# Kernel optimization log

Measured on AMD Instinct MI355X. Metric: run time of the kernel, lower is better.

The kernel has to match this reference:

```python
import jax, jax.numpy as jnp
import numpy as np

COST_CLASS, COST_BBOX, COST_GIOU = 1.0, 5.0, 2.0


def _lsa(cost):
    """Rectangular linear sum assignment (minimize), Jonker-Volgenant style.
    Returns (row_ind, col_ind) like scipy.optimize.linear_sum_assignment."""
    c = np.asarray(cost, dtype=np.float64)
    transposed = c.shape[0] > c.shape[1]
    if transposed:
        c = c.T
    n, m = c.shape  # n <= m
    INF = 1e18
    u = np.zeros(n + 1)
    v = np.zeros(m + 1)
    p = np.zeros(m + 1, dtype=np.int64)   # p[j]: row (1-based) matched to col j, 0 = free
    way = np.zeros(m + 1, dtype=np.int64)
    for i in range(1, n + 1):
        p[0] = i
        j0 = 0
        minv = np.full(m + 1, INF)
        used = np.zeros(m + 1, dtype=bool)
        while True:
            used[j0] = True
            i0 = p[j0]
            cur = c[i0 - 1, :] - u[i0] - v[1:]
            mv = minv[1:]
            upd = (~used[1:]) & (cur < mv)
            mv[upd] = cur[upd]
            way[1:][upd] = j0
            masked = np.where(used[1:], INF, mv)
            j1 = int(np.argmin(masked)) + 1
            delta = masked[j1 - 1]
            u[p[used]] += delta
            v[used] -= delta
            minv[1:][~used[1:]] -= delta
            j0 = j1
            if p[j0] == 0:
                break
        while j0:
            j1 = way[j0]
            p[j0] = p[j1]
            j0 = j1
    rows = p[1:] - 1
    cols = np.arange(m)
    keep = rows >= 0
    ri, ci = rows[keep], cols[keep]
    if transposed:
        ri, ci = ci, ri
    order = np.argsort(ri)
    return ri[order], ci[order]


def _solve_blocks(cost, n_per):
    """cost: np [Q, B*n_per]; solve LSA per diagonal block, return 0/1 solution."""
    Q, T = cost.shape
    B = T // n_per
    sol = np.zeros((Q, T), dtype=np.float32)
    for b in range(B):
        ri, ci = _lsa(cost[:, b * n_per:(b + 1) * n_per])
        sol[ri, b * n_per + ci] = 1.0
    return sol


def box_cxcywh_to_xyxy(b):
    cx, cy, w, h = jnp.split(b, 4, axis=-1)
    return jnp.concatenate([cx - 0.5 * w, cy - 0.5 * h, cx + 0.5 * w, cy + 0.5 * h], axis=-1)


def generalized_box_iou(b1, b2):
    # b1: [N,4] xyxy, b2: [M,4] xyxy -> [N,M]
    area1 = (b1[:, 2] - b1[:, 0]) * (b1[:, 3] - b1[:, 1])
    area2 = (b2[:, 2] - b2[:, 0]) * (b2[:, 3] - b2[:, 1])
    lt = jnp.maximum(b1[:, None, :2], b2[None, :, :2])
    rb = jnp.minimum(b1[:, None, 2:], b2[None, :, 2:])
    wh = jnp.clip(rb - lt, 0.0)
    inter = wh[..., 0] * wh[..., 1]
    union = area1[:, None] + area2[None, :] - inter
    iou = inter / union
    ltc = jnp.minimum(b1[:, None, :2], b2[None, :, :2])
    rbc = jnp.maximum(b1[:, None, 2:], b2[None, :, 2:])
    whc = jnp.clip(rbc - ltc, 0.0)
    areac = whc[..., 0] * whc[..., 1]
    return iou - (areac - union) / areac


def build_cost(pred_logits, pred_boxes, tgt_labels, tgt_boxes, n_per):
    B, Q, C = pred_logits.shape
    out_prob = jax.nn.softmax(pred_logits.reshape(B * Q, C), axis=-1)
    out_bbox = pred_boxes.reshape(B * Q, 4)
    cost_class = -out_prob[:, tgt_labels]                                  # [N,T]
    cost_bbox = jnp.sum(jnp.abs(out_bbox[:, None, :] - tgt_boxes[None, :, :]), axis=-1)  # L1 cdist
    cost_giou = -generalized_box_iou(box_cxcywh_to_xyxy(out_bbox), box_cxcywh_to_xyxy(tgt_boxes))
    cm = COST_BBOX * cost_bbox + COST_CLASS * cost_class + COST_GIOU * cost_giou
    cm = cm.reshape(B, Q, B, n_per)
    blocks = cm[jnp.arange(B), :, jnp.arange(B), :]        # diagonal blocks [B,Q,n_per]
    return jnp.transpose(blocks, (1, 0, 2)).reshape(Q, B * n_per)  # hstack -> [Q, T]


def setup_inputs() -> dict:
    key = jax.random.key(0)
    k1, k2, k3, k4 = jax.random.split(key, 4)
    B, Q, C, n_per = 16, 900, 92, 32
    T = B * n_per
    return {
        "pred_logits": jax.random.normal(k1, (B, Q, C), dtype=jnp.float32),
        "pred_boxes": jax.random.uniform(k2, (B, Q, 4), dtype=jnp.float32),
        "tgt_labels": jax.random.randint(k3, (T,), 0, C, dtype=jnp.int64),
        "tgt_boxes": jax.random.uniform(k4, (T, 4), dtype=jnp.float32),
        "n_targets": n_per,
    }


def reference(pred_logits, pred_boxes, tgt_labels, tgt_boxes, n_targets):
    n_per = int(n_targets)
    cost = build_cost(pred_logits, pred_boxes, tgt_labels, tgt_boxes, n_per)
    sol = jax.pure_callback(
        lambda c: _solve_blocks(np.asarray(c, dtype=np.float64), n_per),
        jax.ShapeDtypeStruct(cost.shape, jnp.float32),
        cost,
    )
    return sol
```

## Files before the change

### kernel.cpp

```cpp
#include <hip/hip_runtime.h>
#include <math.h>

#define BB 16
#define QQ 900
#define CC 92
#define NP 32
#define TT (BB*NP)
#define RSTRIDE 1024
#define NT 512

#define WSC_COST 0
#define WSC_MAX  (BB*NP*RSTRIDE*4)
#define WSC_SUM  (WSC_MAX + BB*QQ*4)
#define WSC_A    (WSC_SUM + BB*QQ*4)
#define WS_NEED  (WSC_A + TT*4)

__device__ __forceinline__ double mkdbl(int lo, int hi) {
    return __longlong_as_double(((long long)hi << 32) | (unsigned int)lo);
}
__device__ __forceinline__ double readlane_dbl(double x, int s) {
    long long l = __double_as_longlong(x);
    int lo = __builtin_amdgcn_readlane((int)l, s);
    int hi = __builtin_amdgcn_readlane((int)(l >> 32), s);
    return mkdbl(lo, hi);
}
__device__ __forceinline__ double bpermute_dbl(int srclane, double x) {
    long long l = __double_as_longlong(x);
    int lo = __builtin_amdgcn_ds_bpermute(srclane << 2, (int)l);
    int hi = __builtin_amdgcn_ds_bpermute(srclane << 2, (int)(l >> 32));
    return mkdbl(lo, hi);
}

#define DPP_MIN64(CTRL)                                                       \
    {                                                                         \
        long long _l = __double_as_longlong(m);                               \
        int _lo = (int)_l, _hi = (int)(_l >> 32);                             \
        int _olo = __builtin_amdgcn_update_dpp(_lo, _lo, CTRL, 0xf, 0xf, false); \
        int _ohi = __builtin_amdgcn_update_dpp(_hi, _hi, CTRL, 0xf, 0xf, false); \
        m = fmin(m, mkdbl(_olo, _ohi));                                       \
    }

__launch_bounds__(256)
__global__ void denom_kernel(const float* __restrict__ logits,
                             float* __restrict__ wmax,
                             float* __restrict__ wsum)
{
    int idx = blockIdx.x * 256 + threadIdx.x;
    if (idx >= BB * QQ) return;
    const float4* row4 = (const float4*)(logits + (size_t)idx * CC);
    float mx = -INFINITY;
    #pragma unroll
    for (int k = 0; k < 23; ++k) {
        float4 x = row4[k];
        mx = fmaxf(mx, x.x); mx = fmaxf(mx, x.y);
        mx = fmaxf(mx, x.z); mx = fmaxf(mx, x.w);
    }
    float s = 0.f;
    #pragma unroll
    for (int k = 0; k < 23; ++k) {
        float4 x = row4[k];
        s += expf(x.x - mx); s += expf(x.y - mx);
        s += expf(x.z - mx); s += expf(x.w - mx);
    }
    wmax[idx] = mx;
    wsum[idx] = s;
}

__launch_bounds__(256)
__global__ void cost_kernel(const float* __restrict__ logits,
                            const float* __restrict__ pboxes,
                            const int*   __restrict__ labels,
                            const float* __restrict__ tboxes,
                            const float* __restrict__ wmax,
                            const float* __restrict__ wsum,
                            float* __restrict__ wcost)
{
    const int r = blockIdx.x;
    const int b = r >> 5, t = r & 31;
    const float* lg = logits + (size_t)b * QQ * CC;
    const float* pb = pboxes + (size_t)b * QQ * 4;
    const float* tb = tboxes + (size_t)b * NP * 4;
    const float* smax = wmax + b * QQ;
    const float* ssum = wsum + b * QQ;

    const float t0 = tb[t*4+0], t1 = tb[t*4+1], t2 = tb[t*4+2], t3 = tb[t*4+3];
    const int   lt = labels[b * NP + t];
    const float tx1 = t0 - 0.5f*t2, ty1 = t1 - 0.5f*t3;
    const float tx2 = t0 + 0.5f*t2, ty2 = t1 + 0.5f*t3;
    const float area2 = (tx2-tx1)*(ty2-ty1);

    float* crow = wcost + (size_t)r * RSTRIDE;
    for (int q = threadIdx.x; q < RSTRIDE; q += 256) {
        float val = 0.f;
        if (q < QQ) {
            float l    = lg[q * CC + lt];
            float prob = expf(l - smax[q]) / ssum[q];
            float cclass = -prob;
            float p0 = pb[q*4+0], p1 = pb[q*4+1], p2 = pb[q*4+2], p3 = pb[q*4+3];
            float cbbox = fabsf(p0-t0) + fabsf(p1-t1)
                        + fabsf(p2-t2) + fabsf(p3-t3);
            float px1 = p0 - 0.5f*p2, py1 = p1 - 0.5f*p3;
            float px2 = p0 + 0.5f*p2, py2 = p1 + 0.5f*p3;
            float area1 = (px2-px1)*(py2-py1);
            float ltx = fmaxf(px1,tx1), lty = fmaxf(py1,ty1);
            float rbx = fminf(px2,tx2), rby = fminf(py2,ty2);
            float wx = fmaxf(rbx-ltx, 0.f), wy = fmaxf(rby-lty, 0.f);
            float inter = wx*wy;
            float uni = area1 + area2 - inter;
            float iou = inter / uni;
            float cx1 = fminf(px1,tx1), cy1 = fminf(py1,ty1);
            float cx2 = fmaxf(px2,tx2), cy2 = fmaxf(py2,ty2);
            float cwx = fmaxf(cx2-cx1, 0.f), cwy = fmaxf(cy2-cy1, 0.f);
            float areac = cwx*cwy;
            float giou = iou - (areac - uni) / areac;
            val = 5.f*cbbox + 1.f*cclass + 2.f*(-giou);
        }
        crow[q] = val;
    }
}

#define C_OFF_COST 0
#define C_SZ_COST  (NP * RSTRIDE * 4)
#define C_OFF_V    (C_OFF_COST + C_SZ_COST)
#define C_OFF_FLAG (C_OFF_V + 7208)
#define C_OFF_ASN  (C_OFF_FLAG + 128)
#define C_DYN      (C_OFF_ASN + 128)

__launch_bounds__(512)
__global__ void walk_kernel(const float* __restrict__ wcost,
                            float* __restrict__ out)
{
    extern __shared__ char smem[];
    float*  s_cost = (float*)(smem + C_OFF_COST);
    double* s_v    = (double*)(smem + C_OFF_V);
    volatile int* s_flag = (volatile int*)(smem + C_OFF_FLAG);
    int*    s_asn  = (int*)(smem + C_OFF_ASN);

    const int b    = blockIdx.x;
    const int tid  = threadIdx.x;
    const int wv   = tid >> 6;
    const int lane = tid & 63;

    if (tid < 32) s_flag[tid] = 0;
    __syncthreads();

    if (wv != 0) {
        for (int t = wv - 1; t < NP; t += 7) {
            const float4* src =
                (const float4*)(wcost + ((size_t)(b * NP + t) * RSTRIDE));
            float4* dst = (float4*)(s_cost + t * RSTRIDE);
            float4 v0 = src[lane];
            float4 v1 = src[lane + 64];
            float4 v2 = src[lane + 128];
            float4 v3 = src[lane + 192];
            dst[lane]       = v0;
            dst[lane + 64]  = v1;
            dst[lane + 128] = v2;
            dst[lane + 192] = v3;
            asm volatile("s_waitcnt vmcnt(0) lgkmcnt(0)" ::: "memory");
            if (lane == 0) s_flag[t] = 1;
        }
    } else {
        for (int j = lane; j <= QQ; j += 64) s_v[j] = 0.0;
        asm volatile("s_waitcnt lgkmcnt(0)" ::: "memory");

        int acol = 0;
        double ureg = 0.0;
        const float4* cbase4 = (const float4*)s_cost;

        double vreg[16];
        #pragma unroll
        for (int k = 0; k < 16; ++k) {
            int col = 4 * lane + ((k >> 2) << 8) + (k & 3) + 1;
            vreg[k] = (col <= QQ) ? 0.0 : -1.0e300;
        }

        int nv = 0;

        while (nv < 1) {
            if (s_flag[0]) nv = 1;
            else __builtin_amdgcn_s_sleep(2);
        }
        float4 cf[4];
        {
            const float4* crow4 = cbase4;
            #pragma unroll
            for (int k = 0; k < 4; ++k) cf[k] = crow4[lane + (k << 6)];
        }

        for (int i = 1; i <= NP; ++i) {
            int i0 = i, j1prev = 0, T = 0;
            int path_reg = 1, row_reg = 1;

            for (int t = 1;; ++t) {
                if (lane == t) row_reg = i0;
                if (j1prev) {
                    #pragma unroll
                    for (int k = 0; k < 16; ++k) {
                        int col = 4 * lane + ((k >> 2) << 8) + (k & 3) + 1;
                        if (col == j1prev) vreg[k] = -1.0e300;
                    }
                }

                double key[16];
                #pragma unroll
                for (int k = 0; k < 4; ++k) {
                    const float* cp = (const float*)&cf[k];
                    #pragma unroll
                    for (int e2 = 0; e2 < 4; ++e2) {
                        int kk  = 4 * k + e2;
                        int col = 4 * lane + (k << 8) + e2 + 1;
                        double d = (double)cp[e2] - vreg[kk];
                        long long bits =
                            (__double_as_longlong(d) & ~2047LL) | (long long)col;
                        key[kk] = __longlong_as_double(bits);
                    }
                }
                double a0 = fmin(key[0], key[1]),   a1 = fmin(key[2], key[3]);
                double a2 = fmin(key[4], key[5]),   a3 = fmin(key[6], key[7]);
                double a4 = fmin(key[8], key[9]),   a5 = fmin(key[10], key[11]);
                double a6 = fmin(key[12], key[13]), a7 = fmin(key[14], key[15]);
                double b0 = fmin(a0, a1), b1 = fmin(a2, a3);
                double b2 = fmin(a4, a5), b3 = fmin(a6, a7);
                double m  = fmin(fmin(b0, b1), fmin(b2, b3));

                DPP_MIN64(0x111);
                DPP_MIN64(0x112);
                DPP_MIN64(0x114);
                DPP_MIN64(0x118);
                DPP_MIN64(0x142);
                DPP_MIN64(0x143);

                int wlo = __builtin_amdgcn_readlane((int)__double_as_longlong(m), 63);
                int j1  = wlo & 2047;

                if (lane == t) path_reg = j1;

                unsigned long long mask = __ballot(acol == j1);
                if (mask == 0) { T = t; break; }
                int L = (int)__builtin_ctzll(mask);
                i0 = L + 1;
                j1prev = j1;

                const float4* crow4 = cbase4 + (size_t)L * (RSTRIDE / 4);
                #pragma unroll
                for (int k = 0; k < 4; ++k) cf[k] = crow4[lane + (k << 6)];
            }

            bool pre = false;
            if (i < NP) {
                if (nv > i) pre = true;
                else if (s_flag[25] && s_flag[26] && s_flag[27] && s_flag[28]
                      && s_flag[29] && s_flag[30] && s_flag[31]) {
                    nv = NP;
                    pre = true;
                }
                if (pre) {
                    const float4* crow4 = cbase4 + (size_t)i * (RSTRIDE / 4);
                    #pragma unroll
                    for (int k = 0; k < 4; ++k) cf[k] = crow4[lane + (k << 6)];
                }
            }

            const int  rt  = row_reg;
            const int  myj = path_reg;
            const bool act = (lane >= 1 && lane <= T);
            double mydelta = 0.0, vv = 0.0;
            {
                double cD = 0.0, v0j = 0.0;
                if (act) {
                    cD  = (double)s_cost[(rt - 1) * RSTRIDE + (myj - 1)];
                    v0j = s_v[myj];
                }
                double u0rt = bpermute_dbl(rt, ureg);
                if (act) {
                    mydelta = (cD - u0rt) - v0j;
                    vv = v0j;
                }
            }
            bool inpath = false;
            for (int s = 1; s <= T; ++s) {
                double ds = readlane_dbl(mydelta, s);
                int    js = __builtin_amdgcn_readlane(path_reg, s);
                int    rs = __builtin_amdgcn_readlane(row_reg, s);
                if (lane + 1 == rs) inpath = true;
                if (inpath) ureg += ds;
                if (lane >= 1 && lane <  s) vv -= ds;
                if (rs == lane + 1) acol = js;
            }
            if (T > 1) {
                if (act) s_v[myj] = vv;
                for (int s = 1; s <= T; ++s) {
                    int    js  = __builtin_amdgcn_readlane(path_reg, s);
                    double vvs = readlane_dbl(vv, s);
                    #pragma unroll
                    for (int k = 0; k < 16; ++k) {
                        int col = 4 * lane + ((k >> 2) << 8) + (k & 3) + 1;
                        if (col == js) vreg[k] = vvs;
                    }
                }
            }

            if (i < NP && !pre) {
                while (nv <= i) {
                    if (s_flag[nv]) ++nv;
                    else __builtin_amdgcn_s_sleep(2);
                }
                const float4* crow4 = cbase4 + (size_t)i * (RSTRIDE / 4);
                #pragma unroll
                for (int k = 0; k < 4; ++k) cf[k] = crow4[lane + (k << 6)];
            }
        }

        if (lane < NP) s_asn[lane] = acol - 1;
    }
    __syncthreads();

    for (int e = tid; e < QQ * 8; e += 512) {
        int q = e >> 3;
        int f = e & 7;
        int base = 4 * f;
        int a0 = s_asn[base + 0], a1 = s_asn[base + 1];
        int a2 = s_asn[base + 2], a3 = s_asn[base + 3];
        float4 o;
        o.x = (a0 == q) ? 1.f : 0.f;
        o.y = (a1 == q) ? 1.f : 0.f;
        o.z = (a2 == q) ? 1.f : 0.f;
        o.w = (a3 == q) ? 1.f : 0.f;
        ((float4*)(out + (size_t)q * TT + b * NP))[f] = o;
    }
}

#define OFF_COST 0
#define SZ_COST  (NP * RSTRIDE * 4)
#define OFF_U    (OFF_COST + SZ_COST)
#define OFF_V    (OFF_U + 264)
#define OFF_P    (OFF_V + 7208)
#define OFF_MAX  (OFF_P + 3604)
#define OFF_SUM  (OFF_MAX + 3600)
#define OFF_FLAG (OFF_SUM + 3600)
#define DYN_BYTES (OFF_FLAG + 128)

__launch_bounds__(NT)
__global__ void matcher_kernel(const float* __restrict__ logits,
                               const float* __restrict__ pboxes,
                               const int*   __restrict__ labels,
                               const float* __restrict__ tboxes,
                               float* __restrict__ out)
{
    extern __shared__ char smem[];
    float*  s_cost = (float*)(smem + OFF_COST);
    double* s_u    = (double*)(smem + OFF_U);
    double* s_v    = (double*)(smem + OFF_V);
    int*    s_p    = (int*)(smem + OFF_P);
    float*  s_max  = (float*)(smem + OFF_MAX);
    float*  s_sum  = (float*)(smem + OFF_SUM);
    volatile int* s_flag = (volatile int*)(smem + OFF_FLAG);

    const int b    = blockIdx.x;
    const int tid  = threadIdx.x;
    const int wv   = tid >> 6;
    const int lane = tid & 63;

    const float* lg = logits + (size_t)b * QQ * CC;
    if (tid < 32) s_flag[tid] = 0;
    for (int q = tid; q < QQ; q += NT) {
        const float4* row4 = (const float4*)(lg + q * CC);
        float mx = -INFINITY;
        #pragma unroll
        for (int k = 0; k < 23; ++k) {
            float4 x = row4[k];
            mx = fmaxf(mx, x.x); mx = fmaxf(mx, x.y);
            mx = fmaxf(mx, x.z); mx = fmaxf(mx, x.w);
        }
        float s = 0.f;
        #pragma unroll
        for (int k = 0; k < 23; ++k) {
            float4 x = row4[k];
            s += expf(x.x - mx); s += expf(x.y - mx);
            s += expf(x.z - mx); s += expf(x.w - mx);
        }
        s_max[q] = mx;
        s_sum[q] = s;
    }
    __syncthreads();

    const float* pb = pboxes + (size_t)b * QQ * 4;
    const float* tb = tboxes + (size_t)b * NP * 4;
    const int*   lb = labels + b * NP;

    if (wv != 0) {
        for (int t = wv - 1; t < NP; t += 7) {
            const float t0 = tb[t*4+0], t1 = tb[t*4+1],
                        t2 = tb[t*4+2], t3 = tb[t*4+3];
            const int   lt = lb[t];
            const float tx1 = t0 - 0.5f*t2, ty1 = t1 - 0.5f*t3;
            const float tx2 = t0 + 0.5f*t2, ty2 = t1 + 0.5f*t3;
            const float area2 = (tx2-tx1)*(ty2-ty1);
            #pragma unroll 4
            for (int it = 0; it < 16; ++it) {
                int q = (it << 6) + lane;
                float val = 0.f;
                if (q < QQ) {
                    float l    = lg[q * CC + lt];
                    float prob = expf(l - s_max[q]) / s_sum[q];
                    float cclass = -prob;
                    float p0 = pb[q*4+0], p1 = pb[q*4+1],
                          p2 = pb[q*4+2], p3 = pb[q*4+3];
                    float cbbox = fabsf(p0-t0) + fabsf(p1-t1)
                                + fabsf(p2-t2) + fabsf(p3-t3);
                    float px1 = p0 - 0.5f*p2, py1 = p1 - 0.5f*p3;
                    float px2 = p0 + 0.5f*p2, py2 = p1 + 0.5f*p3;
                    float area1 = (px2-px1)*(py2-py1);
                    float ltx = fmaxf(px1,tx1), lty = fmaxf(py1,ty1);
                    float rbx = fminf(px2,tx2), rby = fminf(py2,ty2);
                    float wx = fmaxf(rbx-ltx, 0.f), wy = fmaxf(rby-lty, 0.f);
                    float inter = wx*wy;
                    float uni = area1 + area2 - inter;
                    float iou = inter / uni;
                    float cx1 = fminf(px1,tx1), cy1 = fminf(py1,ty1);
                    float cx2 = fmaxf(px2,tx2), cy2 = fmaxf(py2,ty2);
                    float cwx = fmaxf(cx2-cx1, 0.f), cwy = fmaxf(cy2-cy1, 0.f);
                    float areac = cwx*cwy;
                    float giou = iou - (areac - uni) / areac;
                    val = 5.f*cbbox + 1.f*cclass + 2.f*(-giou);
                }
                s_cost[t * RSTRIDE + q] = val;
            }
            asm volatile("s_waitcnt lgkmcnt(0)" ::: "memory");
            if (lane == 0) s_flag[t] = 1;
        }
    } else {
        for (int j = lane; j <= QQ; j += 64) { s_p[j] = 0; s_v[j] = 0.0; }
        if (lane <= NP) s_u[lane] = 0.0;
        asm volatile("s_waitcnt lgkmcnt(0)" ::: "memory");

        int acol = 0;
        const float4* cbase4 = (const float4*)s_cost;

        double vreg[16];
        #pragma unroll
        for (int k = 0; k < 16; ++k) vreg[k] = 0.0;

        unsigned used0 = 0;
        #pragma unroll
        for (int k = 0; k < 16; ++k) {
            int col = 4 * lane + ((k >> 2) << 8) + (k & 3) + 1;
            if (col > QQ) used0 |= 1u << k;
        }

        int nv = 0;
        for (int i = 1; i <= NP; ++i) {
            while (nv < i) {
                if (s_flag[nv]) ++nv;
                else __builtin_amdgcn_s_sleep(2);
            }
            unsigned used = used0;
            int i0 = i, j1prev = 0, T = 0;
            int path_reg = 1, row_reg = 1;
            float4 cf[4];
            {
                const float4* crow4 = cbase4 + (size_t)(i0 - 1) * (RSTRIDE / 4);
                #pragma unroll
                for (int k = 0; k < 4; ++k) cf[k] = crow4[lane + (k << 6)];
            }
            for (int t = 1;; ++t) {
                if (lane == t) row_reg = i0;
                if (j1prev) {
                    int qp = j1prev - 1;
                    if (((qp >> 2) & 63) == lane)
                        used |= 1u << (((qp >> 8) << 2) | (qp & 3));
                }
                double key[16];
                #pragma unroll
                for (int k = 0; k < 4; ++k) {
                    const float* cp = (const float*)&cf[k];
                    #pragma unroll
                    for (int e2 = 0; e2 < 4; ++e2) {
                        int kk  = 4 * k + e2;
                        int col = 4 * lane + (k << 8) + e2 + 1;
                        double d = (double)cp[e2] - vreg[kk];
                        long long bits =
                            (__double_as_longlong(d) & ~2047LL) | (long long)col;
                        key[kk] = ((used >> kk) & 1u)
                                      ? 1e300 : __longlong_as_double(bits);
                    }
                }
                double a0 = fmin(key[0], key[1]),   a1 = fmin(key[2], key[3]);
                double a2 = fmin(key[4], key[5]),   a3 = fmin(key[6], key[7]);
                double a4 = fmin(key[8], key[9]),   a5 = fmin(key[10], key[11]);
                double a6 = fmin(key[12], key[13]), a7 = fmin(key[14], key[15]);
                double b0 = fmin(a0, a1), b1 = fmin(a2, a3);
                double b2 = fmin(a4, a5), b3 = fmin(a6, a7);
                double m  = fmin(fmin(b0, b1), fmin(b2, b3));
                DPP_MIN64(0x111); DPP_MIN64(0x112); DPP_MIN64(0x114);
                DPP_MIN64(0x118); DPP_MIN64(0x142); DPP_MIN64(0x143);
                int wlo = __builtin_amdgcn_readlane((int)__double_as_longlong(m), 63);
                int j1  = wlo & 2047;
                if (lane == t) path_reg = j1;
                unsigned long long mask = __ballot(acol == j1);
                if (mask == 0) { T = t; break; }
                int L = (int)__builtin_ctzll(mask);
                i0 = L + 1;
                j1prev = j1;
                const float4* crow4 = cbase4 + (size_t)L * (RSTRIDE / 4);
                #pragma unroll
                for (int k = 0; k < 4; ++k) cf[k] = crow4[lane + (k << 6)];
            }
            const int  rt  = row_reg;
            const int  myj = path_reg;
            const bool act = (lane >= 1 && lane <= T);
            double mydelta = 0.0, uu = 0.0, vv = 0.0;
            if (act) {
                double cD = (double)s_cost[(rt - 1) * RSTRIDE + (myj - 1)];
                mydelta = (cD - s_u[rt]) - s_v[myj];
                uu = s_u[rt];
                vv = s_v[myj];
            }
            for (int s = 1; s <= T; ++s) {
                double ds = readlane_dbl(mydelta, s);
                int    js = __builtin_amdgcn_readlane(path_reg, s);
                int    rs = __builtin_amdgcn_readlane(row_reg, s);
                if (lane >= 1 && lane <= s) uu += ds;
                if (lane >= 1 && lane <  s) vv -= ds;
                if (rs == lane + 1) acol = js;
            }
            if (act) {
                s_u[rt]  = uu;
                s_v[myj] = vv;
                s_p[myj] = rt;
            }
            for (int s = 1; s <= T; ++s) {
                int    js  = __builtin_amdgcn_readlane(path_reg, s);
                double vvs = readlane_dbl(vv, s);
                #pragma unroll
                for (int k = 0; k < 16; ++k) {
                    int col = 4 * lane + ((k >> 2) << 8) + (k & 3) + 1;
                    if (col == js) vreg[k] = vvs;
                }
            }
        }
    }
    __syncthreads();

    for (int e = tid; e < QQ * 8; e += NT) {
        int q = e >> 3;
        int f = e & 7;
        int pq = s_p[q + 1];
        int base = 4 * f;
        float4 o;
        o.x = (pq == base + 1) ? 1.f : 0.f;
        o.y = (pq == base + 2) ? 1.f : 0.f;
        o.z = (pq == base + 3) ? 1.f : 0.f;
        o.w = (pq == base + 4) ? 1.f : 0.f;
        ((float4*)(out + (size_t)q * TT + b * NP))[f] = o;
    }
}

extern "C" void kernel_launch(void* const* d_in, const int* in_sizes, int n_in,
                              void* d_out, int out_size, void* d_ws, size_t ws_size,
                              hipStream_t stream) {
    const float* logits = (const float*)d_in[0];
    const float* pboxes = (const float*)d_in[1];
    const int*   labels = (const int*)  d_in[2];
    const float* tboxes = (const float*)d_in[3];
    float* out = (float*)d_out;

    if (d_ws != nullptr && ws_size >= (size_t)WS_NEED) {
        float* wcost = (float*)((char*)d_ws + WSC_COST);
        float* wmax  = (float*)((char*)d_ws + WSC_MAX);
        float* wsum  = (float*)((char*)d_ws + WSC_SUM);

        (void)hipFuncSetAttribute((const void*)walk_kernel,
                                  hipFuncAttributeMaxDynamicSharedMemorySize,
                                  C_DYN);

        denom_kernel<<<(BB*QQ + 255)/256, 256, 0, stream>>>(logits, wmax, wsum);
        cost_kernel<<<BB*NP, 256, 0, stream>>>(logits, pboxes, labels, tboxes,
                                               wmax, wsum, wcost);
        walk_kernel<<<BB, 512, C_DYN, stream>>>(wcost, out);
    } else {
        (void)hipFuncSetAttribute((const void*)matcher_kernel,
                                  hipFuncAttributeMaxDynamicSharedMemorySize,
                                  DYN_BYTES);
        matcher_kernel<<<BB, NT, DYN_BYTES, stream>>>(logits, pboxes, labels,
                                                      tboxes, out);
    }
}
```

Before: 98.96 us.

## Read cost rows from global memory and pack two batches per walk block

The walk kernel no longer stages each batch's cost block into shared memory behind flags. The serial auction wave now reads cost rows straight from global memory (kept warm in cache by helper waves that issue discard loads), and each block handles two batches with two solver waves. This drops the shared-memory staging, the flag polling and the dynamic shared allocation, and halves the grid. In exchange every row fetch in the critical serial loop pays global/L2 latency instead of LDS latency, though the next row is now prefetched earlier.

```diff
diff --git a/kernel.cpp b/kernel.cpp
--- a/kernel.cpp
+++ b/kernel.cpp
@@ -119,54 +119,43 @@
     }
 }
 
-#define C_OFF_COST 0
-#define C_SZ_COST  (NP * RSTRIDE * 4)
-#define C_OFF_V    (C_OFF_COST + C_SZ_COST)
-#define C_OFF_FLAG (C_OFF_V + 7208)
-#define C_OFF_ASN  (C_OFF_FLAG + 128)
-#define C_DYN      (C_OFF_ASN + 128)
-
 __launch_bounds__(512)
 __global__ void walk_kernel(const float* __restrict__ wcost,
                             float* __restrict__ out)
 {
-    extern __shared__ char smem[];
-    float*  s_cost = (float*)(smem + C_OFF_COST);
-    double* s_v    = (double*)(smem + C_OFF_V);
-    volatile int* s_flag = (volatile int*)(smem + C_OFF_FLAG);
-    int*    s_asn  = (int*)(smem + C_OFF_ASN);
-
-    const int b    = blockIdx.x;
+    __shared__ double s_v[2][QQ + 1];
+    __shared__ int    s_asn[2][NP];
+
+    const int b2   = blockIdx.x;
     const int tid  = threadIdx.x;
     const int wv   = tid >> 6;
     const int lane = tid & 63;
 
-    if (tid < 32) s_flag[tid] = 0;
-    __syncthreads();
-
-    if (wv != 0) {
-        for (int t = wv - 1; t < NP; t += 7) {
-            const float4* src =
-                (const float4*)(wcost + ((size_t)(b * NP + t) * RSTRIDE));
-            float4* dst = (float4*)(s_cost + t * RSTRIDE);
-            float4 v0 = src[lane];
-            float4 v1 = src[lane + 64];
-            float4 v2 = src[lane + 128];
-            float4 v3 = src[lane + 192];
-            dst[lane]       = v0;
-            dst[lane + 64]  = v1;
-            dst[lane + 128] = v2;
-            dst[lane + 192] = v3;
-            asm volatile("s_waitcnt vmcnt(0) lgkmcnt(0)" ::: "memory");
-            if (lane == 0) s_flag[t] = 1;
-        }
+    if (wv != 0 && wv != 4) {
+        const int bat   = 2 * b2 + (wv >> 2);
+        const int wslot = (wv & 3) - 1;
+        const float4* src = (const float4*)(wcost + (size_t)bat * NP * RSTRIDE);
+        float acc = 0.f;
+        for (int t = wslot; t < NP; t += 3) {
+            float4 a = src[t * 256 + lane];
+            float4 bq = src[t * 256 + lane + 64];
+            float4 c = src[t * 256 + lane + 128];
+            float4 d = src[t * 256 + lane + 192];
+            acc += a.x + bq.y + c.z + d.w;
+        }
+        asm volatile("" :: "v"(acc));
     } else {
-        for (int j = lane; j <= QQ; j += 64) s_v[j] = 0.0;
+        const int wi  = wv >> 2;
+        const int bat = 2 * b2 + wi;
+        double* sv = s_v[wi];
+        for (int j = lane; j <= QQ; j += 64) sv[j] = 0.0;
         asm volatile("s_waitcnt lgkmcnt(0)" ::: "memory");
+
+        const float*  gbase  = wcost + (size_t)bat * NP * RSTRIDE;
+        const float4* cbase4 = (const float4*)gbase;
 
         int acol = 0;
         double ureg = 0.0;
-        const float4* cbase4 = (const float4*)s_cost;
 
         double vreg[16];
         #pragma unroll
@@ -175,12 +164,6 @@
             vreg[k] = (col <= QQ) ? 0.0 : -1.0e300;
         }
 
-        int nv = 0;
-
-        while (nv < 1) {
-            if (s_flag[0]) nv = 1;
-            else __builtin_amdgcn_s_sleep(2);
-        }
         float4 cf[4];
         {
             const float4* crow4 = cbase4;
@@ -221,8 +204,8 @@
                 double a4 = fmin(key[8], key[9]),   a5 = fmin(key[10], key[11]);
                 double a6 = fmin(key[12], key[13]), a7 = fmin(key[14], key[15]);
                 double b0 = fmin(a0, a1), b1 = fmin(a2, a3);
-                double b2 = fmin(a4, a5), b3 = fmin(a6, a7);
-                double m  = fmin(fmin(b0, b1), fmin(b2, b3));
+                double b2d = fmin(a4, a5), b3 = fmin(a6, a7);
+                double m  = fmin(fmin(b0, b1), fmin(b2d, b3));
 
                 DPP_MIN64(0x111);
                 DPP_MIN64(0x112);
@@ -247,31 +230,19 @@
                 for (int k = 0; k < 4; ++k) cf[k] = crow4[lane + (k << 6)];
             }
 
-            bool pre = false;
-            if (i < NP) {
-                if (nv > i) pre = true;
-                else if (s_flag[25] && s_flag[26] && s_flag[27] && s_flag[28]
-                      && s_flag[29] && s_flag[30] && s_flag[31]) {
-                    nv = NP;
-                    pre = true;
-                }
-                if (pre) {
-                    const float4* crow4 = cbase4 + (size_t)i * (RSTRIDE / 4);
-                    #pragma unroll
-                    for (int k = 0; k < 4; ++k) cf[k] = crow4[lane + (k << 6)];
-                }
-            }
-
             const int  rt  = row_reg;
             const int  myj = path_reg;
             const bool act = (lane >= 1 && lane <= T);
             double mydelta = 0.0, vv = 0.0;
             {
                 double cD = 0.0, v0j = 0.0;
-                if (act) {
-                    cD  = (double)s_cost[(rt - 1) * RSTRIDE + (myj - 1)];
-                    v0j = s_v[myj];
-                }
+                if (act) cD = (double)gbase[(rt - 1) * RSTRIDE + (myj - 1)];
+                if (i < NP) {
+                    const float4* crow4 = cbase4 + (size_t)i * (RSTRIDE / 4);
+                    #pragma unroll
+                    for (int k = 0; k < 4; ++k) cf[k] = crow4[lane + (k << 6)];
+                }
+                if (act) v0j = sv[myj];
                 double u0rt = bpermute_dbl(rt, ureg);
                 if (act) {
                     mydelta = (cD - u0rt) - v0j;
@@ -289,7 +260,7 @@
                 if (rs == lane + 1) acol = js;
             }
             if (T > 1) {
-                if (act) s_v[myj] = vv;
+                if (act) sv[myj] = vv;
                 for (int s = 1; s <= T; ++s) {
                     int    js  = __builtin_amdgcn_readlane(path_reg, s);
                     double vvs = readlane_dbl(vv, s);
@@ -300,34 +271,27 @@
                     }
                 }
             }
-
-            if (i < NP && !pre) {
-                while (nv <= i) {
-                    if (s_flag[nv]) ++nv;
-                    else __builtin_amdgcn_s_sleep(2);
-                }
-                const float4* crow4 = cbase4 + (size_t)i * (RSTRIDE / 4);
-                #pragma unroll
-                for (int k = 0; k < 4; ++k) cf[k] = crow4[lane + (k << 6)];
-            }
-        }
-
-        if (lane < NP) s_asn[lane] = acol - 1;
+        }
+
+        if (lane < NP) s_asn[wi][lane] = acol - 1;
     }
     __syncthreads();
 
-    for (int e = tid; e < QQ * 8; e += 512) {
-        int q = e >> 3;
-        int f = e & 7;
+    for (int e = tid; e < QQ * 16; e += 512) {
+        int q   = e >> 4;
+        int rem = e & 15;
+        int wi  = rem >> 3;
+        int f   = rem & 7;
+        int bat = 2 * b2 + wi;
         int base = 4 * f;
-        int a0 = s_asn[base + 0], a1 = s_asn[base + 1];
-        int a2 = s_asn[base + 2], a3 = s_asn[base + 3];
+        int a0 = s_asn[wi][base + 0], a1 = s_asn[wi][base + 1];
+        int a2 = s_asn[wi][base + 2], a3 = s_asn[wi][base + 3];
         float4 o;
         o.x = (a0 == q) ? 1.f : 0.f;
         o.y = (a1 == q) ? 1.f : 0.f;
         o.z = (a2 == q) ? 1.f : 0.f;
         o.w = (a3 == q) ? 1.f : 0.f;
-        ((float4*)(out + (size_t)q * TT + b * NP))[f] = o;
+        ((float4*)(out + (size_t)q * TT + bat * NP))[f] = o;
     }
 }
 
@@ -571,14 +535,10 @@
         float* wmax  = (float*)((char*)d_ws + WSC_MAX);
         float* wsum  = (float*)((char*)d_ws + WSC_SUM);
 
-        (void)hipFuncSetAttribute((const void*)walk_kernel,
-                                  hipFuncAttributeMaxDynamicSharedMemorySize,
-                                  C_DYN);
-
         denom_kernel<<<(BB*QQ + 255)/256, 256, 0, stream>>>(logits, wmax, wsum);
         cost_kernel<<<BB*NP, 256, 0, stream>>>(logits, pboxes, labels, tboxes,
                                                wmax, wsum, wcost);
-        walk_kernel<<<BB, 512, C_DYN, stream>>>(wcost, out);
+        walk_kernel<<<BB/2, 512, 0, stream>>>(wcost, out);
     } else {
         (void)hipFuncSetAttribute((const void*)matcher_kernel,
                                   hipFuncAttributeMaxDynamicSharedMemorySize,
```

Result: slower. 114.9 us (+16.1%).

## Fuse cost-matrix computation into the assignment walk kernel

Applied to the files above, without the earlier changes.

Removes the separate cost_kernel and its global workspace round trip. The seven producer waves in each walk block now compute cost rows directly into shared memory, setting per-row ready flags that the solver wave already polls. This saves one launch and the global write/read of the cost matrix, and lets cost computation overlap with the solver. The trade-off is that cost work now runs on only 16 blocks of 7 waves each instead of 512 blocks, so the solver may stall if rows arrive too slowly.

```diff
diff --git a/kernel.cpp b/kernel.cpp
--- a/kernel.cpp
+++ b/kernel.cpp
@@ -9,11 +9,9 @@
 #define RSTRIDE 1024
 #define NT 512
 
-#define WSC_COST 0
-#define WSC_MAX  (BB*NP*RSTRIDE*4)
-#define WSC_SUM  (WSC_MAX + BB*QQ*4)
-#define WSC_A    (WSC_SUM + BB*QQ*4)
-#define WS_NEED  (WSC_A + TT*4)
+#define WSD_MAX  0
+#define WSD_SUM  (BB*QQ*4)
+#define WS_NEED  (WSD_SUM + BB*QQ*4)
 
 __device__ __forceinline__ double mkdbl(int lo, int hi) {
     return __longlong_as_double(((long long)hi << 32) | (unsigned int)lo);
@@ -66,75 +64,27 @@
     wsum[idx] = s;
 }
 
-__launch_bounds__(256)
-__global__ void cost_kernel(const float* __restrict__ logits,
-                            const float* __restrict__ pboxes,
-                            const int*   __restrict__ labels,
-                            const float* __restrict__ tboxes,
-                            const float* __restrict__ wmax,
-                            const float* __restrict__ wsum,
-                            float* __restrict__ wcost)
-{
-    const int r = blockIdx.x;
-    const int b = r >> 5, t = r & 31;
-    const float* lg = logits + (size_t)b * QQ * CC;
-    const float* pb = pboxes + (size_t)b * QQ * 4;
-    const float* tb = tboxes + (size_t)b * NP * 4;
-    const float* smax = wmax + b * QQ;
-    const float* ssum = wsum + b * QQ;
-
-    const float t0 = tb[t*4+0], t1 = tb[t*4+1], t2 = tb[t*4+2], t3 = tb[t*4+3];
-    const int   lt = labels[b * NP + t];
-    const float tx1 = t0 - 0.5f*t2, ty1 = t1 - 0.5f*t3;
-    const float tx2 = t0 + 0.5f*t2, ty2 = t1 + 0.5f*t3;
-    const float area2 = (tx2-tx1)*(ty2-ty1);
-
-    float* crow = wcost + (size_t)r * RSTRIDE;
-    for (int q = threadIdx.x; q < RSTRIDE; q += 256) {
-        float val = 0.f;
-        if (q < QQ) {
-            float l    = lg[q * CC + lt];
-            float prob = expf(l - smax[q]) / ssum[q];
-            float cclass = -prob;
-            float p0 = pb[q*4+0], p1 = pb[q*4+1], p2 = pb[q*4+2], p3 = pb[q*4+3];
-            float cbbox = fabsf(p0-t0) + fabsf(p1-t1)
-                        + fabsf(p2-t2) + fabsf(p3-t3);
-            float px1 = p0 - 0.5f*p2, py1 = p1 - 0.5f*p3;
-            float px2 = p0 + 0.5f*p2, py2 = p1 + 0.5f*p3;
-            float area1 = (px2-px1)*(py2-py1);
-            float ltx = fmaxf(px1,tx1), lty = fmaxf(py1,ty1);
-            float rbx = fminf(px2,tx2), rby = fminf(py2,ty2);
-            float wx = fmaxf(rbx-ltx, 0.f), wy = fmaxf(rby-lty, 0.f);
-            float inter = wx*wy;
-            float uni = area1 + area2 - inter;
-            float iou = inter / uni;
-            float cx1 = fminf(px1,tx1), cy1 = fminf(py1,ty1);
-            float cx2 = fmaxf(px2,tx2), cy2 = fmaxf(py2,ty2);
-            float cwx = fmaxf(cx2-cx1, 0.f), cwy = fmaxf(cy2-cy1, 0.f);
-            float areac = cwx*cwy;
-            float giou = iou - (areac - uni) / areac;
-            val = 5.f*cbbox + 1.f*cclass + 2.f*(-giou);
-        }
-        crow[q] = val;
-    }
-}
-
-#define C_OFF_COST 0
-#define C_SZ_COST  (NP * RSTRIDE * 4)
-#define C_OFF_V    (C_OFF_COST + C_SZ_COST)
-#define C_OFF_FLAG (C_OFF_V + 7208)
-#define C_OFF_ASN  (C_OFF_FLAG + 128)
-#define C_DYN      (C_OFF_ASN + 128)
+#define F_OFF_COST 0
+#define F_SZ_COST  (NP * RSTRIDE * 4)
+#define F_OFF_V    (F_OFF_COST + F_SZ_COST)
+#define F_OFF_FLAG (F_OFF_V + 7208)
+#define F_OFF_ASN  (F_OFF_FLAG + 128)
+#define F_DYN      (F_OFF_ASN + 128)
 
 __launch_bounds__(512)
-__global__ void walk_kernel(const float* __restrict__ wcost,
-                            float* __restrict__ out)
+__global__ void fused_kernel(const float* __restrict__ logits,
+                             const float* __restrict__ pboxes,
+                             const int*   __restrict__ labels,
+                             const float* __restrict__ tboxes,
+                             const float* __restrict__ wmax,
+                             const float* __restrict__ wsum,
+                             float* __restrict__ out)
 {
     extern __shared__ char smem[];
-    float*  s_cost = (float*)(smem + C_OFF_COST);
-    double* s_v    = (double*)(smem + C_OFF_V);
-    volatile int* s_flag = (volatile int*)(smem + C_OFF_FLAG);
-    int*    s_asn  = (int*)(smem + C_OFF_ASN);
+    float*  s_cost = (float*)(smem + F_OFF_COST);
+    double* s_v    = (double*)(smem + F_OFF_V);
+    volatile int* s_flag = (volatile int*)(smem + F_OFF_FLAG);
+    int*    s_asn  = (int*)(smem + F_OFF_ASN);
 
     const int b    = blockIdx.x;
     const int tid  = threadIdx.x;
@@ -145,19 +95,51 @@
     __syncthreads();
 
     if (wv != 0) {
+        const float* lg = logits + (size_t)b * QQ * CC;
+        const float* pb = pboxes + (size_t)b * QQ * 4;
+        const float* tb = tboxes + (size_t)b * NP * 4;
+        const int*   lb = labels + b * NP;
+        const float* smax = wmax + b * QQ;
+        const float* ssum = wsum + b * QQ;
+
         for (int t = wv - 1; t < NP; t += 7) {
-            const float4* src =
-                (const float4*)(wcost + ((size_t)(b * NP + t) * RSTRIDE));
-            float4* dst = (float4*)(s_cost + t * RSTRIDE);
-            float4 v0 = src[lane];
-            float4 v1 = src[lane + 64];
-            float4 v2 = src[lane + 128];
-            float4 v3 = src[lane + 192];
-            dst[lane]       = v0;
-            dst[lane + 64]  = v1;
-            dst[lane + 128] = v2;
-            dst[lane + 192] = v3;
-            asm volatile("s_waitcnt vmcnt(0) lgkmcnt(0)" ::: "memory");
+            const float t0 = tb[t*4+0], t1 = tb[t*4+1],
+                        t2 = tb[t*4+2], t3 = tb[t*4+3];
+            const int   lt = lb[t];
+            const float tx1 = t0 - 0.5f*t2, ty1 = t1 - 0.5f*t3;
+            const float tx2 = t0 + 0.5f*t2, ty2 = t1 + 0.5f*t3;
+            const float area2 = (tx2-tx1)*(ty2-ty1);
+            #pragma unroll 4
+            for (int it = 0; it < 16; ++it) {
+                int q = (it << 6) + lane;
+                float val = 0.f;
+                if (q < QQ) {
+                    float l    = lg[q * CC + lt];
+                    float prob = expf(l - smax[q]) / ssum[q];
+                    float cclass = -prob;
+                    float p0 = pb[q*4+0], p1 = pb[q*4+1],
+                          p2 = pb[q*4+2], p3 = pb[q*4+3];
+                    float cbbox = fabsf(p0-t0) + fabsf(p1-t1)
+                                + fabsf(p2-t2) + fabsf(p3-t3);
+                    float px1 = p0 - 0.5f*p2, py1 = p1 - 0.5f*p3;
+                    float px2 = p0 + 0.5f*p2, py2 = p1 + 0.5f*p3;
+                    float area1 = (px2-px1)*(py2-py1);
+                    float ltx = fmaxf(px1,tx1), lty = fmaxf(py1,ty1);
+                    float rbx = fminf(px2,tx2), rby = fminf(py2,ty2);
+                    float wx = fmaxf(rbx-ltx, 0.f), wy = fmaxf(rby-lty, 0.f);
+                    float inter = wx*wy;
+                    float uni = area1 + area2 - inter;
+                    float iou = inter / uni;
+                    float cx1 = fminf(px1,tx1), cy1 = fminf(py1,ty1);
+                    float cx2 = fmaxf(px2,tx2), cy2 = fmaxf(py2,ty2);
+                    float cwx = fmaxf(cx2-cx1, 0.f), cwy = fmaxf(cy2-cy1, 0.f);
+                    float areac = cwx*cwy;
+                    float giou = iou - (areac - uni) / areac;
+                    val = 5.f*cbbox + 1.f*cclass + 2.f*(-giou);
+                }
+                s_cost[t * RSTRIDE + q] = val;
+            }
+            asm volatile("s_waitcnt lgkmcnt(0)" ::: "memory");
             if (lane == 0) s_flag[t] = 1;
         }
     } else {
@@ -567,18 +549,16 @@
     float* out = (float*)d_out;
 
     if (d_ws != nullptr && ws_size >= (size_t)WS_NEED) {
-        float* wcost = (float*)((char*)d_ws + WSC_COST);
-        float* wmax  = (float*)((char*)d_ws + WSC_MAX);
-        float* wsum  = (float*)((char*)d_ws + WSC_SUM);
-
-        (void)hipFuncSetAttribute((const void*)walk_kernel,
+        float* wmax = (float*)((char*)d_ws + WSD_MAX);
+        float* wsum = (float*)((char*)d_ws + WSD_SUM);
+
+        (void)hipFuncSetAttribute((const void*)fused_kernel,
                                   hipFuncAttributeMaxDynamicSharedMemorySize,
-                                  C_DYN);
+                                  F_DYN);
 
         denom_kernel<<<(BB*QQ + 255)/256, 256, 0, stream>>>(logits, wmax, wsum);
-        cost_kernel<<<BB*NP, 256, 0, stream>>>(logits, pboxes, labels, tboxes,
-                                               wmax, wsum, wcost);
-        walk_kernel<<<BB, 512, C_DYN, stream>>>(wcost, out);
+        fused_kernel<<<BB, 512, F_DYN, stream>>>(logits, pboxes, labels,
+                                                 tboxes, wmax, wsum, out);
     } else {
         (void)hipFuncSetAttribute((const void*)matcher_kernel,
                                   hipFuncAttributeMaxDynamicSharedMemorySize,
```

Result: slower. 105.6 us (+6.7%).
